# Kernel optimization log

Measured on AMD Instinct MI355X. Metric: run time of the kernel, lower is better.

## Reference

```python
import jax, jax.numpy as jnp
import numpy as np

D_MODEL = 1024
NUM_HEADS = 16
HEAD_DIM = D_MODEL // NUM_HEADS  # 64
# NOTE: the torch module passes scale=attention_head_size (NOT 1/sqrt(dh));
# we reproduce that exact math: scores are MULTIPLIED by head_dim.
SCALE = float(HEAD_DIM)

B, S = 2, 2048


def setup_inputs() -> dict:
    key = jax.random.key(0)
    ks = jax.random.split(key, 6)
    q = jax.random.normal(ks[0], (B, S, D_MODEL), dtype=jnp.float32)
    k = jax.random.normal(ks[1], (B, S, D_MODEL), dtype=jnp.float32)
    v = jax.random.normal(ks[2], (B, S, D_MODEL), dtype=jnp.float32)
    # Linear weights stored as [in, out]; scaled like typical init so the
    # (head_dim-scaled) logits stay numerically sane.
    w_std = 0.02
    Wq = jax.random.normal(ks[3], (D_MODEL, D_MODEL), dtype=jnp.float32) * w_std
    Wk = jax.random.normal(ks[4], (D_MODEL, D_MODEL), dtype=jnp.float32) * w_std
    Wv = jax.random.normal(ks[5], (D_MODEL, D_MODEL), dtype=jnp.float32) * w_std
    return {"q": q, "k": k, "v": v, "Wq": Wq, "Wk": Wk, "Wv": Wv}


def reference(q, k, v, Wq, Wk, Wv):
    Bq, Sq, _ = q.shape
    # QKV projections (qkv_bias=False), split into heads: [B, S, H, dh]
    qh = (q @ Wq).reshape(Bq, Sq, NUM_HEADS, HEAD_DIM)
    kh = (k @ Wk).reshape(Bq, Sq, NUM_HEADS, HEAD_DIM)
    vh = (v @ Wv).reshape(Bq, Sq, NUM_HEADS, HEAD_DIM)
    # Full materialized scores [B, H, Sq, Sk] -- the naive MHA pattern.
    sims = jnp.einsum("bqhd,bkhd->bhqk", qh, kh) * SCALE
    attn = jax.nn.softmax(sims, axis=-1)
    # Second matmul, then merge heads back: [B, S, D]
    out = jnp.einsum("bhqk,bkhd->bqhd", attn, vh).reshape(Bq, Sq, D_MODEL)
    return out
```

## Files before the change

### kernel.cpp

```cpp
#include <hip/hip_runtime.h>
#include <cstdint>
#include <cstddef>

typedef unsigned short u16;
typedef __bf16 bf16x8 __attribute__((ext_vector_type(8)));
typedef float f32x4 __attribute__((ext_vector_type(4)));
typedef unsigned int u32x4 __attribute__((ext_vector_type(4)));
typedef unsigned int u32x2 __attribute__((ext_vector_type(2)));
typedef u16 u16x4 __attribute__((ext_vector_type(4)));

typedef __attribute__((address_space(3))) void lds_void;
typedef __attribute__((address_space(1))) void glb_void;

constexpr float CEXP = 92.33248261689366f;

constexpr size_t XSZ = 4096ull * 1024ull;
constexpr size_t WSZ = 1024ull * 1024ull;
constexpr size_t OFF_XQH = 0;
constexpr size_t OFF_XQL = OFF_XQH + XSZ;
constexpr size_t OFF_XKH = OFF_XQL + XSZ;
constexpr size_t OFF_XKL = OFF_XKH + XSZ;
constexpr size_t OFF_XVH = OFF_XKL + XSZ;
constexpr size_t OFF_XVL = OFF_XVH + XSZ;
constexpr size_t OFF_WQH = OFF_XVL + XSZ;
constexpr size_t OFF_WQL = OFF_WQH + WSZ;
constexpr size_t OFF_WKH = OFF_WQL + WSZ;
constexpr size_t OFF_WKL = OFF_WKH + WSZ;
constexpr size_t OFF_WVH = OFF_WKL + WSZ;
constexpr size_t OFF_WVL = OFF_WVH + WSZ;
constexpr size_t OFF_QH  = OFF_WVL + WSZ;
constexpr size_t OFF_QL  = OFF_QH + XSZ;
constexpr size_t OFF_KH  = OFF_QL + XSZ;
constexpr size_t OFF_KL  = OFF_KH + XSZ;
constexpr size_t OFF_VT  = OFF_KL + XSZ;

__device__ __forceinline__ u16 f2b(float f) {
  unsigned u = __builtin_bit_cast(unsigned, f);
  return (u16)((u + 0x7FFFu + ((u >> 16) & 1u)) >> 16);
}
__device__ __forceinline__ float b2f(u16 h) {
  return __builtin_bit_cast(float, ((unsigned)h) << 16);
}
__device__ __forceinline__ bf16x8 ld8(const u16* p) {
  return __builtin_bit_cast(bf16x8, *(const u32x4*)p);
}
__device__ __forceinline__ unsigned pk2(float a, float b) {
#if __has_builtin(__builtin_amdgcn_cvt_pk_bf16_f32)
  auto v = __builtin_amdgcn_cvt_pk_bf16_f32(a, b);
  return __builtin_bit_cast(unsigned, v);
#else
  return (unsigned)f2b(a) | ((unsigned)f2b(b) << 16);
#endif
}
__device__ __forceinline__ void glds16(const u16* g, u16* l) {
  __builtin_amdgcn_global_load_lds((const glb_void*)g, (lds_void*)l, 16, 0, 0);
}
__device__ __forceinline__ int swz32(int row, int cg) {
  return row * 32 + ((cg ^ ((row >> 1) & 3)) * 8);
}
__device__ __forceinline__ int swz64(int row, int cg) {
  return row * 64 + ((cg ^ (row & 7)) * 8);
}

__global__ __launch_bounds__(256) void convert_x3(const float* __restrict__ q,
                                                  const float* __restrict__ k,
                                                  const float* __restrict__ v,
                                                  u16* __restrict__ ws) {
  int z = blockIdx.y;
  const float* in = (z == 0) ? q : (z == 1) ? k : v;
  u16* hi = ws + ((z == 0) ? OFF_XQH : (z == 1) ? OFF_XKH : OFF_XVH);
  u16* lo = ws + ((z == 0) ? OFF_XQL : (z == 1) ? OFF_XKL : OFF_XVL);
  size_t i = ((size_t)blockIdx.x * 256u + threadIdx.x) * 4u;
  float4 vv = *(const float4*)(in + i);
  float a[4] = {vv.x, vv.y, vv.z, vv.w};
  u16x4 hv, lv;
#pragma unroll
  for (int j = 0; j < 4; ++j) {
    u16 hb = f2b(a[j]);
    hv[j] = hb;
    lv[j] = f2b(a[j] - b2f(hb));
  }
  *(u16x4*)(hi + i) = hv;
  *(u16x4*)(lo + i) = lv;
}

__global__ __launch_bounds__(256) void convert_w3(const float* __restrict__ Wq,
                                                  const float* __restrict__ Wk,
                                                  const float* __restrict__ Wv,
                                                  u16* __restrict__ ws) {
  int z = blockIdx.z;
  const float* W = (z == 0) ? Wq : (z == 1) ? Wk : Wv;
  u16* hiT = ws + ((z == 0) ? OFF_WQH : (z == 1) ? OFF_WKH : OFF_WVH);
  u16* loT = ws + ((z == 0) ? OFF_WQL : (z == 1) ? OFF_WKL : OFF_WVL);
  __shared__ float tile[32][33];
  int n0 = blockIdx.x * 32, k0 = blockIdx.y * 32;
  int t = threadIdx.x;
  int r = t >> 3, c0 = (t & 7) * 4;
  float4 v = *(const float4*)(W + (size_t)(k0 + r) * 1024 + n0 + c0);
  tile[r][c0] = v.x; tile[r][c0 + 1] = v.y; tile[r][c0 + 2] = v.z; tile[r][c0 + 3] = v.w;
  __syncthreads();
  u16x4 hv, lv;
#pragma unroll
  for (int j = 0; j < 4; ++j) {
    float x = tile[c0 + j][r];
    u16 hb = f2b(x);
    hv[j] = hb;
    lv[j] = f2b(x - b2f(hb));
  }
  size_t o = (size_t)(n0 + r) * 1024 + k0 + c0;
  *(u16x4*)(hiT + o) = hv;
  *(u16x4*)(loT + o) = lv;
}

__global__ __launch_bounds__(256) void gemm_qkv(u16* __restrict__ ws) {
  __shared__ u16 lah[128 * 32];
  __shared__ u16 lal[128 * 32];
  __shared__ u16 lbh[128 * 32];
  __shared__ u16 lbl[128 * 32];
  int z = blockIdx.z;
  const u16 *Ah, *Al, *Bh, *Bl; u16 *Oh, *Ol; bool split;
  if (z == 0)      { Ah = ws + OFF_XQH; Al = ws + OFF_XQL; Bh = ws + OFF_WQH; Bl = ws + OFF_WQL; Oh = ws + OFF_QH; Ol = ws + OFF_QL; split = true; }
  else if (z == 1) { Ah = ws + OFF_XKH; Al = ws + OFF_XKL; Bh = ws + OFF_WKH; Bl = ws + OFF_WKL; Oh = ws + OFF_KH; Ol = ws + OFF_KL; split = true; }
  else             { Ah = ws + OFF_XVH; Al = ws + OFF_XVH; Bh = ws + OFF_WVH; Bl = ws + OFF_WVH; Oh = ws + OFF_VT; Ol = nullptr;    split = false; }
  float oscale = (z == 0) ? CEXP : 1.0f;
  int m0 = blockIdx.y * 128, n0 = blockIdx.x * 128;
  int t = threadIdx.x, lane = t & 63, wave = t >> 6;
  int wm = (wave >> 1) * 64, wn = (wave & 1) * 64;
  int rl = lane >> 2, cgl = lane & 3;
  f32x4 acc[4][4] = {};
  for (int kb = 0; kb < 32; ++kb) {
    int k0 = kb * 32;
    __syncthreads();
#pragma unroll
    for (int i = 0; i < 2; ++i) {
      int row = wave * 32 + i * 16 + rl;
      int cgg = cgl ^ ((row >> 1) & 3);
      size_t ga = (size_t)(m0 + row) * 1024 + k0 + cgg * 8;
      size_t gb = (size_t)(n0 + row) * 1024 + k0 + cgg * 8;
      int lbase = (wave * 32 + i * 16) * 32;
      glds16(Ah + ga, &lah[lbase]);
      glds16(Bh + gb, &lbh[lbase]);
      if (split) {
        glds16(Al + ga, &lal[lbase]);
        glds16(Bl + gb, &lbl[lbase]);
      }
    }
    __syncthreads();
    int cg0 = lane >> 4;
    bf16x8 afh[4], afl[4], bfh[4], bfl[4];
#pragma unroll
    for (int i = 0; i < 4; ++i) {
      int ra = wm + i * 16 + (lane & 15);
      int rb = wn + i * 16 + (lane & 15);
      afh[i] = ld8(&lah[swz32(ra, cg0)]);
      bfh[i] = ld8(&lbh[swz32(rb, cg0)]);
      if (split) {
        afl[i] = ld8(&lal[swz32(ra, cg0)]);
        bfl[i] = ld8(&lbl[swz32(rb, cg0)]);
      }
    }
#pragma unroll
    for (int mt = 0; mt < 4; ++mt)
#pragma unroll
      for (int nt = 0; nt < 4; ++nt) {
        acc[mt][nt] = __builtin_amdgcn_mfma_f32_16x16x32_bf16(afh[mt], bfh[nt], acc[mt][nt], 0, 0, 0);
        if (split) {
          acc[mt][nt] = __builtin_amdgcn_mfma_f32_16x16x32_bf16(afl[mt], bfh[nt], acc[mt][nt], 0, 0, 0);
          acc[mt][nt] = __builtin_amdgcn_mfma_f32_16x16x32_bf16(afh[mt], bfl[nt], acc[mt][nt], 0, 0, 0);
        }
      }
  }
  if (z == 2) {
#pragma unroll
    for (int mt = 0; mt < 4; ++mt)
#pragma unroll
      for (int nt = 0; nt < 4; ++nt) {
        int s_base = m0 + wm + mt * 16 + (lane >> 4) * 4;
        int gn = n0 + wn + nt * 16 + (lane & 15);
        int bb = s_base >> 11, s = s_base & 2047, hh = gn >> 6, d = gn & 63;
        u16x4 hv;
#pragma unroll
        for (int r = 0; r < 4; ++r) hv[r] = f2b(acc[mt][nt][r]);
        *(u16x4*)(Oh + ((size_t)((bb * 16 + hh) * 64 + d)) * 2048 + s) = hv;
      }
  } else {
#pragma unroll
    for (int mt = 0; mt < 4; ++mt)
#pragma unroll
      for (int nt = 0; nt < 4; ++nt)
#pragma unroll
        for (int r = 0; r < 4; ++r) {
          int gm = m0 + wm + mt * 16 + (lane >> 4) * 4 + r;
          int gn = n0 + wn + nt * 16 + (lane & 15);
          int bb = gm >> 11, s = gm & 2047, hh = gn >> 6, d = gn & 63;
          size_t oi = ((size_t)(bb * 16 + hh) * 2048 + s) * 64 + d;
          float val = acc[mt][nt][r] * oscale;
          u16 hb = f2b(val);
          Oh[oi] = hb;
          Ol[oi] = f2b(val - b2f(hb));
        }
  }
}

__global__ __launch_bounds__(256) void attn(const u16* __restrict__ ws,
                                            float* __restrict__ out) {
  __shared__ u16 lkh[2][64 * 64];
  __shared__ u16 lkl[2][64 * 64];
  __shared__ u16 lvt[2][64 * 64];
  __shared__ u16 lp[4][16 * 64];
  const u16* Qh = ws + OFF_QH; const u16* Ql = ws + OFF_QL;
  const u16* Kh = ws + OFF_KH; const u16* Kl = ws + OFF_KL;
  const u16* Vt = ws + OFF_VT;
  int b = blockIdx.z, h = blockIdx.y;
  int q0 = blockIdx.x * 64;
  int t = threadIdx.x, lane = t & 63, wave = t >> 6;
  int quad = lane >> 4, l15 = lane & 15;
  size_t hb = (size_t)(b * 16 + h) * (2048 * 64);
  bf16x8 onesf;
#pragma unroll
  for (int j = 0; j < 8; ++j) onesf[j] = __builtin_bit_cast(__bf16, (u16)0x3F80);
  int qrow = q0 + wave * 16 + l15;
  bf16x8 qfh[2], qfl[2];
#pragma unroll
  for (int ks = 0; ks < 2; ++ks) {
    size_t qo = hb + (size_t)qrow * 64 + ks * 32 + quad * 8;
    qfh[ks] = ld8(Qh + qo);
    qfl[ks] = ld8(Ql + qo);
  }
  float mi = -1e30f;
  f32x4 lsum = {};
  f32x4 o[4] = {};
  int rl = lane >> 3, cgl = lane & 7;

  auto stage = [&](int kt, int bsel) {
#pragma unroll
    for (int i = 0; i < 2; ++i) {
      int row = wave * 16 + i * 8 + rl;
      int cgg = cgl ^ (row & 7);
      int lbase = (wave * 16 + i * 8) * 64;
      size_t gk = hb + (size_t)(kt * 64 + row) * 64 + cgg * 8;
      glds16(Kh + gk, &lkh[bsel][lbase]);
      glds16(Kl + gk, &lkl[bsel][lbase]);
      size_t gv = hb + (size_t)row * 2048 + kt * 64 + cgg * 8;
      glds16(Vt + gv, &lvt[bsel][lbase]);
    }
  };

  stage(0, 0);
  __syncthreads();

  for (int kt = 0; kt < 32; ++kt) {
    int cur = kt & 1;
    stage((kt + 1) & 31, cur ^ 1);
    f32x4 sc[4] = {};
#pragma unroll
    for (int nt = 0; nt < 4; ++nt) {
#pragma unroll
      for (int ks = 0; ks < 2; ++ks) {
        int so = swz64(nt * 16 + l15, ks * 4 + quad);
        bf16x8 kh_ = ld8(&lkh[cur][so]);
        bf16x8 kl_ = ld8(&lkl[cur][so]);
        sc[nt] = __builtin_amdgcn_mfma_f32_16x16x32_bf16(kh_, qfh[ks], sc[nt], 0, 0, 0);
        sc[nt] = __builtin_amdgcn_mfma_f32_16x16x32_bf16(kl_, qfh[ks], sc[nt], 0, 0, 0);
        sc[nt] = __builtin_amdgcn_mfma_f32_16x16x32_bf16(kh_, qfl[ks], sc[nt], 0, 0, 0);
      }
    }
    float mx = fmaxf(fmaxf(fmaxf(sc[0][0], sc[0][1]), fmaxf(sc[0][2], sc[0][3])),
                     fmaxf(fmaxf(sc[1][0], sc[1][1]), fmaxf(sc[1][2], sc[1][3])));
    float mx2 = fmaxf(fmaxf(fmaxf(sc[2][0], sc[2][1]), fmaxf(sc[2][2], sc[2][3])),
                      fmaxf(fmaxf(sc[3][0], sc[3][1]), fmaxf(sc[3][2], sc[3][3])));
    mx = fmaxf(mx, mx2);
    mx = fmaxf(mx, __shfl_xor(mx, 16));
    mx = fmaxf(mx, __shfl_xor(mx, 32));
    float mn = fmaxf(mi, mx);
    float alpha_s = exp2f(mi - mn);
    mi = mn;
    u16* lpw = &lp[wave][0];
    int r7 = l15 & 7;
#pragma unroll
    for (int nt = 0; nt < 4; ++nt) {
      float e0 = exp2f(sc[nt][0] - mn);
      float e1 = exp2f(sc[nt][1] - mn);
      float e2 = exp2f(sc[nt][2] - mn);
      float e3 = exp2f(sc[nt][3] - mn);
      unsigned u01 = pk2(e0, e1), u23 = pk2(e2, e3);
      int c = nt * 2 + (quad >> 1);
      int off = l15 * 64 + ((c ^ r7) * 8) + (quad & 1) * 4;
      *(u32x2*)(&lpw[off]) = u32x2{u01, u23};
    }
    float av[4];
#pragma unroll
    for (int r = 0; r < 4; ++r) av[r] = __shfl(alpha_s, quad * 4 + r);
#pragma unroll
    for (int r = 0; r < 4; ++r) {
      lsum[r] *= av[r];
      o[0][r] *= av[r]; o[1][r] *= av[r]; o[2][r] *= av[r]; o[3][r] *= av[r];
    }
    asm volatile("s_waitcnt lgkmcnt(0)" ::: "memory");
    bf16x8 pa[2];
#pragma unroll
    for (int ks = 0; ks < 2; ++ks)
      pa[ks] = ld8(&lpw[swz64(l15, ks * 4 + quad)]);
    lsum = __builtin_amdgcn_mfma_f32_16x16x32_bf16(pa[0], onesf, lsum, 0, 0, 0);
    lsum = __builtin_amdgcn_mfma_f32_16x16x32_bf16(pa[1], onesf, lsum, 0, 0, 0);
#pragma unroll
    for (int nt = 0; nt < 4; ++nt)
#pragma unroll
      for (int ks = 0; ks < 2; ++ks) {
        bf16x8 bv = ld8(&lvt[cur][swz64(nt * 16 + l15, ks * 4 + quad)]);
        o[nt] = __builtin_amdgcn_mfma_f32_16x16x32_bf16(pa[ks], bv, o[nt], 0, 0, 0);
      }
    __syncthreads();
  }
  float inv[4];
#pragma unroll
  for (int r = 0; r < 4; ++r) inv[r] = 1.0f / lsum[r];
#pragma unroll
  for (int nt = 0; nt < 4; ++nt)
#pragma unroll
    for (int r = 0; r < 4; ++r) {
      int srow = q0 + wave * 16 + quad * 4 + r;
      int d = nt * 16 + l15;
      out[(size_t)(b * 2048 + srow) * 1024 + h * 64 + d] = o[nt][r] * inv[r];
    }
}

extern "C" void kernel_launch(void* const* d_in, const int* in_sizes, int n_in,
                              void* d_out, int out_size, void* d_ws, size_t ws_size,
                              hipStream_t stream) {
  const float* q  = (const float*)d_in[0];
  const float* k  = (const float*)d_in[1];
  const float* v  = (const float*)d_in[2];
  const float* Wq = (const float*)d_in[3];
  const float* Wk = (const float*)d_in[4];
  const float* Wv = (const float*)d_in[5];
  u16* ws = (u16*)d_ws;
  float* out = (float*)d_out;

  convert_x3<<<dim3(4096, 3), 256, 0, stream>>>(q, k, v, ws);
  convert_w3<<<dim3(32, 32, 3), 256, 0, stream>>>(Wq, Wk, Wv, ws);
  gemm_qkv<<<dim3(8, 32, 3), 256, 0, stream>>>(ws);
  attn<<<dim3(32, 16, 2), 256, 0, stream>>>(ws, out);
}
```

Before: 312.9 us.

## Drop attention double buffering, raise occupancy, hoist address math, use fast exp2

New measurement: 379.8 us. 1.21x slower.

```diff
diff --git a/kernel.cpp b/kernel.cpp
--- a/kernel.cpp
+++ b/kernel.cpp
@@ -52,6 +52,13 @@
   return (unsigned)f2b(a) | ((unsigned)f2b(b) << 16);
 #endif
 }
+__device__ __forceinline__ float ex2(float x) {
+#if __has_builtin(__builtin_amdgcn_exp2f)
+  return __builtin_amdgcn_exp2f(x);
+#else
+  return exp2f(x);
+#endif
+}
 __device__ __forceinline__ void glds16(const u16* g, u16* l) {
   __builtin_amdgcn_global_load_lds((const glb_void*)g, (lds_void*)l, 16, 0, 0);
 }
@@ -112,7 +119,7 @@
   *(u16x4*)(loT + o) = lv;
 }
 
-__global__ __launch_bounds__(256) void gemm_qkv(u16* __restrict__ ws) {
+__global__ __launch_bounds__(256, 4) void gemm_qkv(u16* __restrict__ ws) {
   __shared__ u16 lah[128 * 32];
   __shared__ u16 lal[128 * 32];
   __shared__ u16 lbh[128 * 32];
@@ -128,21 +135,25 @@
   int wm = (wave >> 1) * 64, wn = (wave & 1) * 64;
   int rl = lane >> 2, cgl = lane & 3;
   f32x4 acc[4][4] = {};
+  size_t gA[2], gB[2]; int lb[2];
+#pragma unroll
+  for (int i = 0; i < 2; ++i) {
+    int row = wave * 32 + i * 16 + rl;
+    int cgg = cgl ^ ((row >> 1) & 3);
+    gA[i] = (size_t)(m0 + row) * 1024 + cgg * 8;
+    gB[i] = (size_t)(n0 + row) * 1024 + cgg * 8;
+    lb[i] = (wave * 32 + i * 16) * 32;
+  }
   for (int kb = 0; kb < 32; ++kb) {
     int k0 = kb * 32;
     __syncthreads();
 #pragma unroll
     for (int i = 0; i < 2; ++i) {
-      int row = wave * 32 + i * 16 + rl;
-      int cgg = cgl ^ ((row >> 1) & 3);
-      size_t ga = (size_t)(m0 + row) * 1024 + k0 + cgg * 8;
-      size_t gb = (size_t)(n0 + row) * 1024 + k0 + cgg * 8;
-      int lbase = (wave * 32 + i * 16) * 32;
-      glds16(Ah + ga, &lah[lbase]);
-      glds16(Bh + gb, &lbh[lbase]);
+      glds16(Ah + gA[i] + k0, &lah[lb[i]]);
+      glds16(Bh + gB[i] + k0, &lbh[lb[i]]);
       if (split) {
-        glds16(Al + ga, &lal[lbase]);
-        glds16(Bl + gb, &lbl[lbase]);
+        glds16(Al + gA[i] + k0, &lal[lb[i]]);
+        glds16(Bl + gB[i] + k0, &lbl[lb[i]]);
       }
     }
     __syncthreads();
@@ -202,11 +213,11 @@
   }
 }
 
-__global__ __launch_bounds__(256) void attn(const u16* __restrict__ ws,
-                                            float* __restrict__ out) {
-  __shared__ u16 lkh[2][64 * 64];
-  __shared__ u16 lkl[2][64 * 64];
-  __shared__ u16 lvt[2][64 * 64];
+__global__ __launch_bounds__(256, 4) void attn(const u16* __restrict__ ws,
+                                               float* __restrict__ out) {
+  __shared__ u16 lkh[64 * 64];
+  __shared__ u16 lkl[64 * 64];
+  __shared__ u16 lvt[64 * 64];
   __shared__ u16 lp[4][16 * 64];
   const u16* Qh = ws + OFF_QH; const u16* Ql = ws + OFF_QL;
   const u16* Kh = ws + OFF_KH; const u16* Kl = ws + OFF_KL;
@@ -232,34 +243,51 @@
   f32x4 o[4] = {};
   int rl = lane >> 3, cgl = lane & 7;
 
-  auto stage = [&](int kt, int bsel) {
+  size_t aK[2], aV[2]; int lb[2];
+#pragma unroll
+  for (int i = 0; i < 2; ++i) {
+    int row = wave * 16 + i * 8 + rl;
+    int cgg = cgl ^ (row & 7);
+    aK[i] = hb + (size_t)row * 64 + cgg * 8;
+    aV[i] = hb + (size_t)row * 2048 + cgg * 8;
+    lb[i] = (wave * 16 + i * 8) * 64;
+  }
+  int soF[2][4];
+#pragma unroll
+  for (int ks = 0; ks < 2; ++ks)
+#pragma unroll
+    for (int nt = 0; nt < 4; ++nt)
+      soF[ks][nt] = swz64(nt * 16 + l15, ks * 4 + quad);
+  int soP[4];
+  {
+    int r7 = l15 & 7;
+#pragma unroll
+    for (int nt = 0; nt < 4; ++nt) {
+      int c = nt * 2 + (quad >> 1);
+      soP[nt] = l15 * 64 + ((c ^ r7) * 8) + (quad & 1) * 4;
+    }
+  }
+  int soPa[2];
+#pragma unroll
+  for (int ks = 0; ks < 2; ++ks) soPa[ks] = swz64(l15, ks * 4 + quad);
+  u16* lpw = &lp[wave][0];
+
+  for (int kt = 0; kt < 32; ++kt) {
+    __syncthreads();
 #pragma unroll
     for (int i = 0; i < 2; ++i) {
-      int row = wave * 16 + i * 8 + rl;
-      int cgg = cgl ^ (row & 7);
-      int lbase = (wave * 16 + i * 8) * 64;
-      size_t gk = hb + (size_t)(kt * 64 + row) * 64 + cgg * 8;
-      glds16(Kh + gk, &lkh[bsel][lbase]);
-      glds16(Kl + gk, &lkl[bsel][lbase]);
-      size_t gv = hb + (size_t)row * 2048 + kt * 64 + cgg * 8;
-      glds16(Vt + gv, &lvt[bsel][lbase]);
-    }
-  };
-
-  stage(0, 0);
-  __syncthreads();
-
-  for (int kt = 0; kt < 32; ++kt) {
-    int cur = kt & 1;
-    stage((kt + 1) & 31, cur ^ 1);
+      glds16(Kh + aK[i] + kt * 4096, &lkh[lb[i]]);
+      glds16(Kl + aK[i] + kt * 4096, &lkl[lb[i]]);
+      glds16(Vt + aV[i] + kt * 64,   &lvt[lb[i]]);
+    }
+    __syncthreads();
     f32x4 sc[4] = {};
 #pragma unroll
     for (int nt = 0; nt < 4; ++nt) {
 #pragma unroll
       for (int ks = 0; ks < 2; ++ks) {
-        int so = swz64(nt * 16 + l15, ks * 4 + quad);
-        bf16x8 kh_ = ld8(&lkh[cur][so]);
-        bf16x8 kl_ = ld8(&lkl[cur][so]);
+        bf16x8 kh_ = ld8(&lkh[soF[ks][nt]]);
+        bf16x8 kl_ = ld8(&lkl[soF[ks][nt]]);
         sc[nt] = __builtin_amdgcn_mfma_f32_16x16x32_bf16(kh_, qfh[ks], sc[nt], 0, 0, 0);
         sc[nt] = __builtin_amdgcn_mfma_f32_16x16x32_bf16(kl_, qfh[ks], sc[nt], 0, 0, 0);
         sc[nt] = __builtin_amdgcn_mfma_f32_16x16x32_bf16(kh_, qfl[ks], sc[nt], 0, 0, 0);
@@ -273,44 +301,37 @@
     mx = fmaxf(mx, __shfl_xor(mx, 16));
     mx = fmaxf(mx, __shfl_xor(mx, 32));
     float mn = fmaxf(mi, mx);
-    float alpha_s = exp2f(mi - mn);
+    float alpha_s = ex2(mi - mn);
     mi = mn;
-    u16* lpw = &lp[wave][0];
-    int r7 = l15 & 7;
 #pragma unroll
     for (int nt = 0; nt < 4; ++nt) {
-      float e0 = exp2f(sc[nt][0] - mn);
-      float e1 = exp2f(sc[nt][1] - mn);
-      float e2 = exp2f(sc[nt][2] - mn);
-      float e3 = exp2f(sc[nt][3] - mn);
-      unsigned u01 = pk2(e0, e1), u23 = pk2(e2, e3);
-      int c = nt * 2 + (quad >> 1);
-      int off = l15 * 64 + ((c ^ r7) * 8) + (quad & 1) * 4;
-      *(u32x2*)(&lpw[off]) = u32x2{u01, u23};
-    }
-    float av[4];
-#pragma unroll
-    for (int r = 0; r < 4; ++r) av[r] = __shfl(alpha_s, quad * 4 + r);
-#pragma unroll
-    for (int r = 0; r < 4; ++r) {
-      lsum[r] *= av[r];
-      o[0][r] *= av[r]; o[1][r] *= av[r]; o[2][r] *= av[r]; o[3][r] *= av[r];
+      unsigned u01 = pk2(ex2(sc[nt][0] - mn), ex2(sc[nt][1] - mn));
+      unsigned u23 = pk2(ex2(sc[nt][2] - mn), ex2(sc[nt][3] - mn));
+      *(u32x2*)(&lpw[soP[nt]]) = u32x2{u01, u23};
+    }
+    if (__ballot(alpha_s != 1.0f)) {
+      float av[4];
+#pragma unroll
+      for (int r = 0; r < 4; ++r) av[r] = __shfl(alpha_s, quad * 4 + r);
+#pragma unroll
+      for (int r = 0; r < 4; ++r) {
+        lsum[r] *= av[r];
+        o[0][r] *= av[r]; o[1][r] *= av[r]; o[2][r] *= av[r]; o[3][r] *= av[r];
+      }
     }
     asm volatile("s_waitcnt lgkmcnt(0)" ::: "memory");
     bf16x8 pa[2];
 #pragma unroll
-    for (int ks = 0; ks < 2; ++ks)
-      pa[ks] = ld8(&lpw[swz64(l15, ks * 4 + quad)]);
+    for (int ks = 0; ks < 2; ++ks) pa[ks] = ld8(&lpw[soPa[ks]]);
     lsum = __builtin_amdgcn_mfma_f32_16x16x32_bf16(pa[0], onesf, lsum, 0, 0, 0);
     lsum = __builtin_amdgcn_mfma_f32_16x16x32_bf16(pa[1], onesf, lsum, 0, 0, 0);
 #pragma unroll
     for (int nt = 0; nt < 4; ++nt)
 #pragma unroll
       for (int ks = 0; ks < 2; ++ks) {
-        bf16x8 bv = ld8(&lvt[cur][swz64(nt * 16 + l15, ks * 4 + quad)]);
+        bf16x8 bv = ld8(&lvt[soF[ks][nt]]);
         o[nt] = __builtin_amdgcn_mfma_f32_16x16x32_bf16(pa[ks], bv, o[nt], 0, 0, 0);
       }
-    __syncthreads();
   }
   float inv[4];
 #pragma unroll
```
